# Kernel tuning notes

Hardware: AMD Instinct MI355X
Metric: run time of the kernel (lower is better)

## Reference

```python
import jax, jax.numpy as jnp
import numpy as np

B = 4096; NA = 32; DIU = 128; DOU = 32; DIB = 256; DOB = 64; DH = 128; N = NA + 1


def setup_inputs() -> dict:
    key = jax.random.key(0)
    ks = jax.random.split(key, 40)
    kidx = [0]
    def rn(shape, scale=0.1):
        k = ks[kidx[0]]; kidx[0] += 1
        return jax.random.normal(k, shape, jnp.float32) * scale
    inp = {}
    inp['s'] = rn((B, DIU * NA + DIB), 1.0)
    inp['a'] = rn((B, DOU * NA + DOB), 1.0)
    for pre, din in (('ue', DIU + DOU), ('bs', DIB + DOB)):
        inp[pre + '_l1_w'] = rn((din, DH))
        inp[pre + '_l1_b'] = jnp.zeros((DH,), jnp.float32)
        inp[pre + '_l2_w'] = rn((DH, DH))
        inp[pre + '_l2_b'] = jnp.zeros((DH,), jnp.float32)
        for l in range(2):
            inp[pre + f'_gru_wih{l}'] = rn((3 * DH, DH))
            inp[pre + f'_gru_whh{l}'] = rn((3 * DH, DH))
            inp[pre + f'_gru_bih{l}'] = jnp.zeros((3 * DH,), jnp.float32)
            inp[pre + f'_gru_bhh{l}'] = jnp.zeros((3 * DH,), jnp.float32)
    inp['gat_w'] = rn((DH, DH))
    inp['gat_a'] = rn((2 * DH, 1))
    adj = np.zeros((N, N), np.float32)
    adj[1:, 0] = 1.0
    adj[0, 1:] = 1.0  # star graph, as in generate_adjacent_matrix
    inp['adj'] = jnp.asarray(adj)
    inp['ev1_w'] = rn((DH, DH))
    inp['ev1_b'] = jnp.zeros((DH,), jnp.float32)
    inp['ev2_w'] = rn((DH, 1))
    inp['ev2_b'] = jnp.zeros((1,), jnp.float32)
    return inp


def _gru_layer(x, wih, whh, bih, bhh):
    # x: [B, T, H]; torch GRU gate order (r, z, n), weights [3H, H]
    h0 = jnp.zeros((x.shape[0], whh.shape[1]), x.dtype)
    def step(h, xt):
        gi = xt @ wih.T + bih
        gh = h @ whh.T + bhh
        ir, iz, inn = jnp.split(gi, 3, axis=-1)
        hr, hz, hn = jnp.split(gh, 3, axis=-1)
        r = jax.nn.sigmoid(ir + hr)
        z = jax.nn.sigmoid(iz + hz)
        n = jnp.tanh(inn + r * hn)
        h_new = (1.0 - z) * n + z * h
        return h_new, h_new
    _, ys = jax.lax.scan(step, h0, jnp.swapaxes(x, 0, 1))
    return jnp.swapaxes(ys, 0, 1)


def _critic(si, ai, l1w, l1b, l2w, l2b, g0, g1):
    x = jax.nn.relu(jnp.concatenate([si, ai], axis=-1) @ l1w + l1b)
    x = jax.nn.sigmoid(x @ l2w + l2b)
    x = _gru_layer(x, *g0)
    x = _gru_layer(x, *g1)
    return x


def reference(s, a,
              ue_l1_w, ue_l1_b, ue_l2_w, ue_l2_b,
              ue_gru_wih0, ue_gru_whh0, ue_gru_bih0, ue_gru_bhh0,
              ue_gru_wih1, ue_gru_whh1, ue_gru_bih1, ue_gru_bhh1,
              bs_l1_w, bs_l1_b, bs_l2_w, bs_l2_b,
              bs_gru_wih0, bs_gru_whh0, bs_gru_bih0, bs_gru_bhh0,
              bs_gru_wih1, bs_gru_whh1, bs_gru_bih1, bs_gru_bhh1,
              gat_w, gat_a, adj, ev1_w, ev1_b, ev2_w, ev2_b):
    batch = s.shape[0]
    s_ue = s[:, :DIU * NA].reshape(batch, NA, DIU)
    s_bs = s[:, DIU * NA:].reshape(batch, 1, DIB)
    a_ue = a[:, :DOU * NA].reshape(batch, NA, DOU)
    a_bs = a[:, -DOB:].reshape(batch, 1, DOB)
    emb_ue = _critic(s_ue, a_ue, ue_l1_w, ue_l1_b, ue_l2_w, ue_l2_b,
                     (ue_gru_wih0, ue_gru_whh0, ue_gru_bih0, ue_gru_bhh0),
                     (ue_gru_wih1, ue_gru_whh1, ue_gru_bih1, ue_gru_bhh1))
    emb_bs = _critic(s_bs, a_bs, bs_l1_w, bs_l1_b, bs_l2_w, bs_l2_b,
                     (bs_gru_wih0, bs_gru_whh0, bs_gru_bih0, bs_gru_bhh0),
                     (bs_gru_wih1, bs_gru_whh1, bs_gru_bih1, bs_gru_bhh1))
    emb = jnp.concatenate([emb_ue, emb_bs], axis=1)  # [B, N, DH]
    # GAT layer
    Wh = emb @ gat_w                                  # [B, N, DH]
    Wh1 = Wh @ gat_a[:DH]                             # [B, N, 1]
    Wh2 = Wh @ gat_a[DH:]                             # [B, N, 1]
    e = jax.nn.leaky_relu(Wh1 + jnp.swapaxes(Wh2, 1, 2), negative_slope=0.01)
    att = jnp.where(adj > 0, e, jnp.float32(-9e15))
    att = jax.nn.softmax(att, axis=1)                 # NOTE: dim=1, as in source
    # dropout is identity in eval mode
    h_prime = jnp.einsum('bij,bjf->bf', att, Wh)      # matmul + sum over dim 1
    h_prime = jax.nn.elu(h_prime)
    x = jax.nn.relu(h_prime @ ev1_w + ev1_b)
    return x @ ev2_w + ev2_b                          # [B, 1]
```

## Files before the change

kernel.cpp:

```cpp
#include <hip/hip_runtime.h>


typedef unsigned short u16;
typedef __bf16  bf16x8  __attribute__((ext_vector_type(8)));
typedef short   short8  __attribute__((ext_vector_type(8)));
typedef u16     u16x4   __attribute__((ext_vector_type(4)));
typedef float   floatx4 __attribute__((ext_vector_type(4)));

#define DEVI __device__ __forceinline__
#define MFMA(a, b, c) __builtin_amdgcn_mfma_f32_16x16x32_bf16((a), (b), (c), 0, 0, 0)

DEVI u16 f2b(float f) {
    unsigned u = __float_as_uint(f);
    u += 0x7fffu + ((u >> 16) & 1u);
    return (u16)(u >> 16);
}
DEVI float b2f(u16 s) { return __uint_as_float(((unsigned)s) << 16); }
DEVI float sigm(float x) { return 1.f / (1.f + __expf(-x)); }
DEVI float tanh_(float x) { return 1.f - 2.f / (__expf(2.f * x) + 1.f); }

DEVI bf16x8 ldfrag(const u16* q) {
    return *reinterpret_cast<const bf16x8*>(q);
}
DEVI bf16x8 ldfrag_f32(const float* q) {
    float4 u = *reinterpret_cast<const float4*>(q);
    float4 v = *reinterpret_cast<const float4*>(q + 4);
    short8 pk;
    pk[0] = (short)f2b(u.x); pk[1] = (short)f2b(u.y);
    pk[2] = (short)f2b(u.z); pk[3] = (short)f2b(u.w);
    pk[4] = (short)f2b(v.x); pk[5] = (short)f2b(v.y);
    pk[6] = (short)f2b(v.z); pk[7] = (short)f2b(v.w);
    return __builtin_bit_cast(bf16x8, pk);
}

enum : int {
    O_UE_W1T  = 0,
    O_UE_W2T  = 20480,
    O_UE_WIH0 = 36864,
    O_UE_WHH0 = 86016,
    O_UE_WIH1 = 135168,
    O_UE_WHH1 = 184320,
    O_BS_W1T  = 233472,
    O_BS_W2T  = 274432,
    O_BS_WIH0 = 290816,
    O_BS_WIH1 = 339968,
    O_GATWT   = 389120,
    O_EV1T    = 405504,
};
#define WB_X2   1048576u
#define WB_Y0   34603008u
#define WB_X2BS 135266304u
#define WB_H0BS 136314880u
#define WB_HBS  137363456u
#define WB_SSUM 139460608u

__global__ __launch_bounds__(256) void k_prep(
    const float* __restrict__ ue1, const float* __restrict__ ue2,
    const float* __restrict__ uw0, const float* __restrict__ uh0,
    const float* __restrict__ uw1, const float* __restrict__ uh1,
    const float* __restrict__ bs1, const float* __restrict__ bs2,
    const float* __restrict__ bw0, const float* __restrict__ bw1,
    const float* __restrict__ gw,  const float* __restrict__ e1,
    u16* __restrict__ out)
{
    const int tid = blockIdx.x * blockDim.x + threadIdx.x;
    const int stride = gridDim.x * blockDim.x;
    auto cvt = [&](const float* s, int off, int n) {
        for (int i = tid; i < n; i += stride) out[off + i] = f2b(s[i]);
    };
    auto tcv = [&](const float* s, int off, int K, int N) {
        const int tot = K * N;
        for (int i = tid; i < tot; i += stride) {
            int nn = i / K, kk = i - nn * K;
            out[off + i] = f2b(s[kk * N + nn]);
        }
    };
    tcv(ue1, O_UE_W1T, 160, 128);  tcv(ue2, O_UE_W2T, 128, 128);
    cvt(uw0, O_UE_WIH0, 49152);    cvt(uh0, O_UE_WHH0, 49152);
    cvt(uw1, O_UE_WIH1, 49152);    cvt(uh1, O_UE_WHH1, 49152);
    tcv(bs1, O_BS_W1T, 320, 128);  tcv(bs2, O_BS_W2T, 128, 128);
    cvt(bw0, O_BS_WIH0, 49152);    cvt(bw1, O_BS_WIH1, 49152);
    tcv(gw,  O_GATWT, 128, 128);   tcv(e1,  O_EV1T, 128, 128);
}

__global__ __launch_bounds__(512, 2) void k_ue_l1l2(
    const float* __restrict__ s, const float* __restrict__ a,
    const u16* __restrict__ W1T, const float* __restrict__ b1,
    const u16* __restrict__ W2T, const float* __restrict__ b2,
    u16* __restrict__ X2)
{
    __shared__ __align__(16) u16 A1[128][168];
    __shared__ __align__(16) u16 H[128][136];
    const int tid = threadIdx.x;
    const int w = tid >> 6, lane = tid & 63;
    const int lm = lane & 15, lg = lane >> 4;
    const int r0 = blockIdx.x * 128;

    bf16x8 bw1[5], bw2[4];
#pragma unroll
    for (int ks = 0; ks < 5; ++ks)
        bw1[ks] = ldfrag(W1T + (w * 16 + lm) * 160 + ks * 32 + lg * 8);
#pragma unroll
    for (int ks = 0; ks < 4; ++ks)
        bw2[ks] = ldfrag(W2T + (w * 16 + lm) * 128 + ks * 32 + lg * 8);
    const float bias1 = b1[w * 16 + lm];
    const float bias2 = b2[w * 16 + lm];

#pragma unroll
    for (int it = 0; it < 8; ++it) {
        const int fidx = it * 512 + tid;
        const int row = fidx >> 5, c4 = fidx & 31;
        const int r = r0 + row, bb = r >> 5, tt = r & 31;
        float4 v = *reinterpret_cast<const float4*>(s + (size_t)bb * 4352 + tt * 128 + c4 * 4);
        u16x4 p = {f2b(v.x), f2b(v.y), f2b(v.z), f2b(v.w)};
        *reinterpret_cast<u16x4*>(&A1[row][c4 * 4]) = p;
    }
#pragma unroll
    for (int it = 0; it < 2; ++it) {
        const int fidx = it * 512 + tid;
        const int row = fidx >> 3, c4 = fidx & 7;
        const int r = r0 + row, bb = r >> 5, tt = r & 31;
        float4 v = *reinterpret_cast<const float4*>(a + (size_t)bb * 1088 + tt * 32 + c4 * 4);
        u16x4 p = {f2b(v.x), f2b(v.y), f2b(v.z), f2b(v.w)};
        *reinterpret_cast<u16x4*>(&A1[row][128 + c4 * 4]) = p;
    }
    __syncthreads();

#pragma unroll
    for (int mt = 0; mt < 8; ++mt) {
        bf16x8 af[5];
#pragma unroll
        for (int ks = 0; ks < 5; ++ks)
            af[ks] = ldfrag(&A1[mt * 16 + lm][ks * 32 + lg * 8]);
        floatx4 acc = {0.f, 0.f, 0.f, 0.f};
#pragma unroll
        for (int ks = 0; ks < 5; ++ks) acc = MFMA(af[ks], bw1[ks], acc);
#pragma unroll
        for (int i = 0; i < 4; ++i) {
            float x = acc[i] + bias1;
            H[mt * 16 + lg * 4 + i][w * 16 + lm] = f2b(x > 0.f ? x : 0.f);
        }
    }
    __syncthreads();

#pragma unroll
    for (int mt = 0; mt < 8; ++mt) {
        bf16x8 af[4];
#pragma unroll
        for (int ks = 0; ks < 4; ++ks)
            af[ks] = ldfrag(&H[mt * 16 + lm][ks * 32 + lg * 8]);
        floatx4 acc = {0.f, 0.f, 0.f, 0.f};
#pragma unroll
        for (int ks = 0; ks < 4; ++ks) acc = MFMA(af[ks], bw2[ks], acc);
#pragma unroll
        for (int i = 0; i < 4; ++i)
            X2[(size_t)(r0 + mt * 16 + lg * 4 + i) * 128 + w * 16 + lm] =
                f2b(sigm(acc[i] + bias2));
    }
}

template <int MODE>
__global__ __launch_bounds__(512, 2) void k_scan(
    const u16* __restrict__ X, const u16* __restrict__ WIH,
    const u16* __restrict__ WHH,
    const float* __restrict__ bih, const float* __restrict__ bhh,
    u16* __restrict__ Y, float* __restrict__ Ssum)
{
    __shared__ __align__(16) u16 hb[2][16][136];
    const int w = threadIdx.x >> 6, lane = threadIdx.x & 63;
    const int lm = lane & 15, lg = lane >> 4;
    const int b0 = blockIdx.x * 16;
    const int c = w * 16 + lm;

    bf16x8 bwh[3][4], bwi[3][4];
#pragma unroll
    for (int g = 0; g < 3; ++g)
#pragma unroll
        for (int ks = 0; ks < 4; ++ks) {
            bwh[g][ks] = ldfrag(WHH + (g * 128 + c) * 128 + ks * 32 + lg * 8);
            bwi[g][ks] = ldfrag(WIH + (g * 128 + c) * 128 + ks * 32 + lg * 8);
        }

    for (int i = threadIdx.x; i < 2 * 16 * 136; i += 512) ((u16*)hb)[i] = 0;

    const float br  = bih[c] + bhh[c];
    const float bz  = bih[128 + c] + bhh[128 + c];
    const float bni = bih[256 + c], bnh = bhh[256 + c];

    const u16* xp = X + (size_t)(b0 + lm) * 32 * 128 + lg * 8;
    bf16x8 xa[4], xn[4];
#pragma unroll
    for (int ks = 0; ks < 4; ++ks) xa[ks] = ldfrag(xp + ks * 32);

    float hreg[4] = {}, ssum[4] = {};
    __syncthreads();

    int cur = 0;
    for (int t = 0; t < 32; ++t) {
        bf16x8 af[4];
#pragma unroll
        for (int ks = 0; ks < 4; ++ks)
            af[ks] = ldfrag(&hb[cur][lm][ks * 32 + lg * 8]);

        floatx4 gacc[3];
#pragma unroll
        for (int g = 0; g < 3; ++g) gacc[g] = floatx4{0.f, 0.f, 0.f, 0.f};
#pragma unroll
        for (int g = 0; g < 3; ++g)
#pragma unroll
            for (int ks = 0; ks < 4; ++ks)
                gacc[g] = MFMA(xa[ks], bwi[g][ks], gacc[g]);

        if (t < 31) {
#pragma unroll
            for (int ks = 0; ks < 4; ++ks)
                xn[ks] = ldfrag(xp + (t + 1) * 128 + ks * 32);
        }

        floatx4 hacc[3];
#pragma unroll
        for (int g = 0; g < 3; ++g) hacc[g] = floatx4{0.f, 0.f, 0.f, 0.f};
#pragma unroll
        for (int g = 0; g < 3; ++g)
#pragma unroll
            for (int ks = 0; ks < 4; ++ks)
                hacc[g] = MFMA(af[ks], bwh[g][ks], hacc[g]);

        const int nxt = cur ^ 1;
#pragma unroll
        for (int i = 0; i < 4; ++i) {
            const float rr = sigm(gacc[0][i] + hacc[0][i] + br);
            const float zz = sigm(gacc[1][i] + hacc[1][i] + bz);
            const float nn = tanh_(gacc[2][i] + bni + rr * (hacc[2][i] + bnh));
            const float hn = (1.f - zz) * nn + zz * hreg[i];
            hreg[i] = hn;
            if (MODE == 1) ssum[i] += hn;
            const u16 hv = f2b(hn);
            hb[nxt][lg * 4 + i][c] = hv;
            if (MODE == 0)
                Y[((size_t)(b0 + lg * 4 + i) * 32 + t) * 128 + c] = hv;
        }
#pragma unroll
        for (int ks = 0; ks < 4; ++ks) xa[ks] = xn[ks];

        __builtin_amdgcn_sched_barrier(0);
        asm volatile("s_waitcnt lgkmcnt(0)" ::: "memory");
        __builtin_amdgcn_s_barrier();
        __builtin_amdgcn_sched_barrier(0);
        cur = nxt;
    }
    if (MODE == 1) {
#pragma unroll
        for (int i = 0; i < 4; ++i)
            Ssum[(size_t)(b0 + lg * 4 + i) * 128 + c] = ssum[i];
    }
}

__global__ __launch_bounds__(256, 2) void k_bs_l1l2(
    const float* __restrict__ s, const float* __restrict__ a,
    const u16* __restrict__ W1T, const float* __restrict__ b1,
    const u16* __restrict__ W2T, const float* __restrict__ b2,
    u16* __restrict__ X2)
{
    __shared__ __align__(16) u16 hb[4][16][136];
    const int w = threadIdx.x >> 6, lane = threadIdx.x & 63;
    const int lm = lane & 15, lg = lane >> 4;
    const int r0 = blockIdx.x * 64 + w * 16;
    const float* srow = s + (size_t)(r0 + lm) * 4352 + 4096 + lg * 8;
    const float* arow = a + (size_t)(r0 + lm) * 1088 + 1024 + lg * 8;

    bf16x8 af[10];
#pragma unroll
    for (int ks = 0; ks < 8; ++ks) af[ks] = ldfrag_f32(srow + ks * 32);
    af[8] = ldfrag_f32(arow);
    af[9] = ldfrag_f32(arow + 32);

    const u16* wb1 = W1T + lm * 320 + lg * 8;
#pragma unroll
    for (int n = 0; n < 8; ++n) {
        floatx4 acc = {0.f, 0.f, 0.f, 0.f};
#pragma unroll
        for (int ks = 0; ks < 10; ++ks)
            acc = MFMA(af[ks], ldfrag(wb1 + n * 5120 + ks * 32), acc);
        const float bias = b1[n * 16 + lm];
#pragma unroll
        for (int i = 0; i < 4; ++i) {
            float x = acc[i] + bias;
            hb[w][lg * 4 + i][n * 16 + lm] = f2b(x > 0.f ? x : 0.f);
        }
    }
    __syncthreads();

    bf16x8 af2[4];
#pragma unroll
    for (int ks = 0; ks < 4; ++ks) af2[ks] = ldfrag(&hb[w][lm][ks * 32 + lg * 8]);
    const u16* wb2 = W2T + lm * 128 + lg * 8;
#pragma unroll
    for (int n = 0; n < 8; ++n) {
        floatx4 acc = {0.f, 0.f, 0.f, 0.f};
#pragma unroll
        for (int ks = 0; ks < 4; ++ks)
            acc = MFMA(af2[ks], ldfrag(wb2 + n * 2048 + ks * 32), acc);
        const float bias = b2[n * 16 + lm];
#pragma unroll
        for (int i = 0; i < 4; ++i) {
            float v = sigm(acc[i] + bias);
            X2[(unsigned)(r0 + lg * 4 + i) * 128u + n * 16 + lm] = f2b(v);
        }
    }
}

template <int OUTF32>
__global__ __launch_bounds__(256, 2) void k_bs_gru(
    const u16* __restrict__ X, const u16* __restrict__ WIH,
    const float* __restrict__ bih, const float* __restrict__ bhh,
    u16* __restrict__ Hb, float* __restrict__ Hf)
{
    const int w = threadIdx.x >> 6, lane = threadIdx.x & 63;
    const int lm = lane & 15, lg = lane >> 4;
    const int r0 = blockIdx.x * 64 + w * 16;

    bf16x8 ax[4];
    const u16* xr = X + (unsigned)(r0 + lm) * 128u + lg * 8;
#pragma unroll
    for (int ks = 0; ks < 4; ++ks) ax[ks] = ldfrag(xr + ks * 32);

    floatx4 acc[24];
#pragma unroll
    for (int j = 0; j < 24; ++j) acc[j] = floatx4{0.f, 0.f, 0.f, 0.f};
    const u16* wbp = WIH + lm * 128 + lg * 8;
#pragma unroll
    for (int j = 0; j < 24; ++j)
#pragma unroll
        for (int ks = 0; ks < 4; ++ks)
            acc[j] = MFMA(ax[ks], ldfrag(wbp + j * 2048 + ks * 32), acc[j]);

#pragma unroll
    for (int ct = 0; ct < 8; ++ct) {
        const int c = ct * 16 + lm;
        const float br = bih[c] + bhh[c];
        const float bz = bih[128 + c] + bhh[128 + c];
        const float bni = bih[256 + c], bnh = bhh[256 + c];
#pragma unroll
        for (int i = 0; i < 4; ++i) {
            const float rr = sigm(acc[ct][i] + br);
            const float zz = sigm(acc[8 + ct][i] + bz);
            const float nn = tanh_(acc[16 + ct][i] + bni + rr * bnh);
            const float h = (1.f - zz) * nn;
            const unsigned row = (unsigned)(r0 + lg * 4 + i);
            if (OUTF32) Hf[row * 128u + c] = h;
            else        Hb[row * 128u + c] = f2b(h);
        }
    }
}

__global__ __launch_bounds__(256, 2) void k_final(
    const float* __restrict__ Ssum, const float* __restrict__ HBS,
    const u16* __restrict__ GATWT, const u16* __restrict__ EV1T,
    const float* __restrict__ ev1b, const float* __restrict__ ev2w,
    const float* __restrict__ ev2b, float* __restrict__ out)
{
    __shared__ __align__(16) u16 hb[4][16][136];
    __shared__ float xb[4][16][132];
    const int w = threadIdx.x >> 6, lane = threadIdx.x & 63;
    const int lm = lane & 15, lg = lane >> 4;
    const int r0 = blockIdx.x * 64 + w * 16;

    const float* p1 = Ssum + (unsigned)(r0 + lm) * 128u + lg * 8;
    const float* p2 = HBS  + (unsigned)(r0 + lm) * 128u + lg * 8;
    bf16x8 af[4];
#pragma unroll
    for (int ks = 0; ks < 4; ++ks) {
        float4 u = *reinterpret_cast<const float4*>(p1 + ks * 32);
        float4 u2 = *reinterpret_cast<const float4*>(p1 + ks * 32 + 4);
        float4 v = *reinterpret_cast<const float4*>(p2 + ks * 32);
        float4 v2 = *reinterpret_cast<const float4*>(p2 + ks * 32 + 4);
        short8 pk;
        pk[0] = (short)f2b(u.x + v.x); pk[1] = (short)f2b(u.y + v.y);
        pk[2] = (short)f2b(u.z + v.z); pk[3] = (short)f2b(u.w + v.w);
        pk[4] = (short)f2b(u2.x + v2.x); pk[5] = (short)f2b(u2.y + v2.y);
        pk[6] = (short)f2b(u2.z + v2.z); pk[7] = (short)f2b(u2.w + v2.w);
        af[ks] = __builtin_bit_cast(bf16x8, pk);
    }
    const u16* gwp = GATWT + lm * 128 + lg * 8;
#pragma unroll
    for (int n = 0; n < 8; ++n) {
        floatx4 acc = {0.f, 0.f, 0.f, 0.f};
#pragma unroll
        for (int ks = 0; ks < 4; ++ks)
            acc = MFMA(af[ks], ldfrag(gwp + n * 2048 + ks * 32), acc);
#pragma unroll
        for (int i = 0; i < 4; ++i) {
            float x = acc[i];
            x = x > 0.f ? x : (__expf(x) - 1.f);
            hb[w][lg * 4 + i][n * 16 + lm] = f2b(x);
        }
    }
    __syncthreads();

    bf16x8 af2[4];
#pragma unroll
    for (int ks = 0; ks < 4; ++ks) af2[ks] = ldfrag(&hb[w][lm][ks * 32 + lg * 8]);
    const u16* e1p = EV1T + lm * 128 + lg * 8;
#pragma unroll
    for (int n = 0; n < 8; ++n) {
        floatx4 acc = {0.f, 0.f, 0.f, 0.f};
#pragma unroll
        for (int ks = 0; ks < 4; ++ks)
            acc = MFMA(af2[ks], ldfrag(e1p + n * 2048 + ks * 32), acc);
        const float bias = ev1b[n * 16 + lm];
#pragma unroll
        for (int i = 0; i < 4; ++i) {
            float v = acc[i] + bias;
            xb[w][lg * 4 + i][n * 16 + lm] = v > 0.f ? v : 0.f;
        }
    }
    __syncthreads();

    float sacc = 0.f;
#pragma unroll
    for (int k = 0; k < 32; ++k) {
        const int c = lg * 32 + k;
        sacc += xb[w][lm][c] * ev2w[c];
    }
    sacc += __shfl_xor(sacc, 16, 64);
    sacc += __shfl_xor(sacc, 32, 64);
    if (lg == 0) out[r0 + lm] = sacc + ev2b[0];
}

extern "C" void kernel_launch(void* const* d_in, const int* in_sizes, int n_in,
                              void* d_out, int out_size, void* d_ws, size_t ws_size,
                              hipStream_t stream)
{
    (void)in_sizes; (void)n_in; (void)out_size; (void)ws_size;
    const float* s       = (const float*)d_in[0];
    const float* a       = (const float*)d_in[1];
    const float* ue_l1_w = (const float*)d_in[2];
    const float* ue_l1_b = (const float*)d_in[3];
    const float* ue_l2_w = (const float*)d_in[4];
    const float* ue_l2_b = (const float*)d_in[5];
    const float* ue_wih0 = (const float*)d_in[6];
    const float* ue_whh0 = (const float*)d_in[7];
    const float* ue_bih0 = (const float*)d_in[8];
    const float* ue_bhh0 = (const float*)d_in[9];
    const float* ue_wih1 = (const float*)d_in[10];
    const float* ue_whh1 = (const float*)d_in[11];
    const float* ue_bih1 = (const float*)d_in[12];
    const float* ue_bhh1 = (const float*)d_in[13];
    const float* bs_l1_w = (const float*)d_in[14];
    const float* bs_l1_b = (const float*)d_in[15];
    const float* bs_l2_w = (const float*)d_in[16];
    const float* bs_l2_b = (const float*)d_in[17];
    const float* bs_wih0 = (const float*)d_in[18];
    const float* bs_bih0 = (const float*)d_in[20];
    const float* bs_bhh0 = (const float*)d_in[21];
    const float* bs_wih1 = (const float*)d_in[22];
    const float* bs_bih1 = (const float*)d_in[24];
    const float* bs_bhh1 = (const float*)d_in[25];
    const float* gat_w   = (const float*)d_in[26];
    const float* ev1_w   = (const float*)d_in[29];
    const float* ev1_b   = (const float*)d_in[30];
    const float* ev2_w   = (const float*)d_in[31];
    const float* ev2_b   = (const float*)d_in[32];

    char* ws = (char*)d_ws;
    u16*   wb   = (u16*)ws;
    u16*   X2   = (u16*)(ws + WB_X2);
    u16*   Y0   = (u16*)(ws + WB_Y0);
    u16*   X2BS = (u16*)(ws + WB_X2BS);
    u16*   H0BS = (u16*)(ws + WB_H0BS);
    float* HBS  = (float*)(ws + WB_HBS);
    float* SSUM = (float*)(ws + WB_SSUM);

    k_prep<<<256, 256, 0, stream>>>(ue_l1_w, ue_l2_w, ue_wih0, ue_whh0,
                                    ue_wih1, ue_whh1, bs_l1_w, bs_l2_w,
                                    bs_wih0, bs_wih1, gat_w, ev1_w, wb);
    k_ue_l1l2<<<1024, 512, 0, stream>>>(s, a, wb + O_UE_W1T, ue_l1_b,
                                        wb + O_UE_W2T, ue_l2_b, X2);
    k_scan<0><<<256, 512, 0, stream>>>(X2, wb + O_UE_WIH0, wb + O_UE_WHH0,
                                       ue_bih0, ue_bhh0, Y0, nullptr);
    k_scan<1><<<256, 512, 0, stream>>>(Y0, wb + O_UE_WIH1, wb + O_UE_WHH1,
                                       ue_bih1, ue_bhh1, nullptr, SSUM);
    k_bs_l1l2<<<64, 256, 0, stream>>>(s, a, wb + O_BS_W1T, bs_l1_b,
                                      wb + O_BS_W2T, bs_l2_b, X2BS);
    k_bs_gru<0><<<64, 256, 0, stream>>>(X2BS, wb + O_BS_WIH0, bs_bih0, bs_bhh0,
                                        H0BS, nullptr);
    k_bs_gru<1><<<64, 256, 0, stream>>>(H0BS, wb + O_BS_WIH1, bs_bih1, bs_bhh1,
                                        nullptr, HBS);
    k_final<<<64, 256, 0, stream>>>(SSUM, HBS, wb + O_GATWT, wb + O_EV1T,
                                    ev1_b, ev2_w, ev2_b, (float*)d_out);
}
```

Measured before the change: 370.6 us.

## Fuse BS critic kernels into final kernel and restructure GRU scan step

Merges the four small BS-path kernels (l1/l2, two single-step GRU layers, final GAT/eval head) into one kernel that keeps intermediates in shared memory instead of round-tripping through global workspace, removing three launches. The scan loop is manually unrolled by two with static ping-pong LDS buffers, input and hidden MFMAs accumulate into shared r/z accumulators, and s_setprio wraps the MFMA section. The added x prefetch depth and shared-memory reuse raise register and LDS pressure and need careful barrier placement.

New measurement: 359.3 us. -3.0%, faster.

```diff
diff --git a/kernel.cpp b/kernel.cpp
--- a/kernel.cpp
+++ b/kernel.cpp
@@ -49,9 +49,6 @@
 };
 #define WB_X2   1048576u
 #define WB_Y0   34603008u
-#define WB_X2BS 135266304u
-#define WB_H0BS 136314880u
-#define WB_HBS  137363456u
 #define WB_SSUM 139460608u
 
 __global__ __launch_bounds__(256) void k_prep(
@@ -159,6 +156,47 @@
     }
 }
 
+#define SCAN_STEP(RBUF, WBUF, XA, TCUR, PREF_T)                               \
+  {                                                                           \
+    bf16x8 af[4];                                                             \
+    _Pragma("unroll") for (int ks = 0; ks < 4; ++ks)                          \
+        af[ks] = ldfrag(&RBUF[lm][ks * 32 + lg * 8]);                         \
+    floatx4 accR{0.f,0.f,0.f,0.f}, accZ{0.f,0.f,0.f,0.f};                     \
+    floatx4 accGN{0.f,0.f,0.f,0.f}, accHN{0.f,0.f,0.f,0.f};                   \
+    __builtin_amdgcn_s_setprio(1);                                            \
+    _Pragma("unroll") for (int ks = 0; ks < 4; ++ks) {                        \
+        accR  = MFMA(XA[ks], bwi[0][ks], accR);                               \
+        accZ  = MFMA(XA[ks], bwi[1][ks], accZ);                               \
+        accGN = MFMA(XA[ks], bwi[2][ks], accGN);                              \
+    }                                                                         \
+    if ((PREF_T) < 32) {                                                      \
+        _Pragma("unroll") for (int ks = 0; ks < 4; ++ks)                      \
+            XA[ks] = ldfrag(xp + (PREF_T) * 128 + ks * 32);                   \
+    }                                                                         \
+    _Pragma("unroll") for (int ks = 0; ks < 4; ++ks) {                        \
+        accR = MFMA(af[ks], bwh[0][ks], accR);                                \
+        accZ = MFMA(af[ks], bwh[1][ks], accZ);                                \
+        accHN = MFMA(af[ks], bwh[2][ks], accHN);                              \
+    }                                                                         \
+    __builtin_amdgcn_s_setprio(0);                                            \
+    _Pragma("unroll") for (int i = 0; i < 4; ++i) {                           \
+        const float rr = sigm(accR[i] + br);                                  \
+        const float zz = sigm(accZ[i] + bz);                                  \
+        const float nn = tanh_(accGN[i] + bni + rr * (accHN[i] + bnh));       \
+        const float hn = (1.f - zz) * nn + zz * hreg[i];                      \
+        hreg[i] = hn;                                                         \
+        if (MODE == 1) ssum[i] += hn;                                         \
+        const u16 hv = f2b(hn);                                               \
+        WBUF[lg * 4 + i][c] = hv;                                             \
+        if (MODE == 0)                                                        \
+            Y[((size_t)(b0 + lg * 4 + i) * 32 + (TCUR)) * 128 + c] = hv;      \
+    }                                                                         \
+    __builtin_amdgcn_sched_barrier(0);                                        \
+    asm volatile("s_waitcnt lgkmcnt(0)" ::: "memory");                        \
+    __builtin_amdgcn_s_barrier();                                             \
+    __builtin_amdgcn_sched_barrier(0);                                        \
+  }
+
 template <int MODE>
 __global__ __launch_bounds__(512, 2) void k_scan(
     const u16* __restrict__ X, const u16* __restrict__ WIH,
@@ -166,7 +204,8 @@
     const float* __restrict__ bih, const float* __restrict__ bhh,
     u16* __restrict__ Y, float* __restrict__ Ssum)
 {
-    __shared__ __align__(16) u16 hb[2][16][136];
+    __shared__ __align__(16) u16 hb0[16][136];
+    __shared__ __align__(16) u16 hb1[16][136];
     const int w = threadIdx.x >> 6, lane = threadIdx.x & 63;
     const int lm = lane & 15, lg = lane >> 4;
     const int b0 = blockIdx.x * 16;
@@ -181,73 +220,28 @@
             bwi[g][ks] = ldfrag(WIH + (g * 128 + c) * 128 + ks * 32 + lg * 8);
         }
 
-    for (int i = threadIdx.x; i < 2 * 16 * 136; i += 512) ((u16*)hb)[i] = 0;
+    for (int i = threadIdx.x; i < 16 * 136; i += 512) {
+        ((u16*)hb0)[i] = 0; ((u16*)hb1)[i] = 0;
+    }
 
     const float br  = bih[c] + bhh[c];
     const float bz  = bih[128 + c] + bhh[128 + c];
     const float bni = bih[256 + c], bnh = bhh[256 + c];
 
     const u16* xp = X + (size_t)(b0 + lm) * 32 * 128 + lg * 8;
-    bf16x8 xa[4], xn[4];
-#pragma unroll
-    for (int ks = 0; ks < 4; ++ks) xa[ks] = ldfrag(xp + ks * 32);
+    bf16x8 xa[4], xb[4];
+#pragma unroll
+    for (int ks = 0; ks < 4; ++ks) {
+        xa[ks] = ldfrag(xp + ks * 32);
+        xb[ks] = ldfrag(xp + 128 + ks * 32);
+    }
 
     float hreg[4] = {}, ssum[4] = {};
     __syncthreads();
 
-    int cur = 0;
-    for (int t = 0; t < 32; ++t) {
-        bf16x8 af[4];
-#pragma unroll
-        for (int ks = 0; ks < 4; ++ks)
-            af[ks] = ldfrag(&hb[cur][lm][ks * 32 + lg * 8]);
-
-        floatx4 gacc[3];
-#pragma unroll
-        for (int g = 0; g < 3; ++g) gacc[g] = floatx4{0.f, 0.f, 0.f, 0.f};
-#pragma unroll
-        for (int g = 0; g < 3; ++g)
-#pragma unroll
-            for (int ks = 0; ks < 4; ++ks)
-                gacc[g] = MFMA(xa[ks], bwi[g][ks], gacc[g]);
-
-        if (t < 31) {
-#pragma unroll
-            for (int ks = 0; ks < 4; ++ks)
-                xn[ks] = ldfrag(xp + (t + 1) * 128 + ks * 32);
-        }
-
-        floatx4 hacc[3];
-#pragma unroll
-        for (int g = 0; g < 3; ++g) hacc[g] = floatx4{0.f, 0.f, 0.f, 0.f};
-#pragma unroll
-        for (int g = 0; g < 3; ++g)
-#pragma unroll
-            for (int ks = 0; ks < 4; ++ks)
-                hacc[g] = MFMA(af[ks], bwh[g][ks], hacc[g]);
-
-        const int nxt = cur ^ 1;
-#pragma unroll
-        for (int i = 0; i < 4; ++i) {
-            const float rr = sigm(gacc[0][i] + hacc[0][i] + br);
-            const float zz = sigm(gacc[1][i] + hacc[1][i] + bz);
-            const float nn = tanh_(gacc[2][i] + bni + rr * (hacc[2][i] + bnh));
-            const float hn = (1.f - zz) * nn + zz * hreg[i];
-            hreg[i] = hn;
-            if (MODE == 1) ssum[i] += hn;
-            const u16 hv = f2b(hn);
-            hb[nxt][lg * 4 + i][c] = hv;
-            if (MODE == 0)
-                Y[((size_t)(b0 + lg * 4 + i) * 32 + t) * 128 + c] = hv;
-        }
-#pragma unroll
-        for (int ks = 0; ks < 4; ++ks) xa[ks] = xn[ks];
-
-        __builtin_amdgcn_sched_barrier(0);
-        asm volatile("s_waitcnt lgkmcnt(0)" ::: "memory");
-        __builtin_amdgcn_s_barrier();
-        __builtin_amdgcn_sched_barrier(0);
-        cur = nxt;
+    for (int tt = 0; tt < 32; tt += 2) {
+        SCAN_STEP(hb0, hb1, xa, tt,     tt + 2);
+        SCAN_STEP(hb1, hb0, xb, tt + 1, tt + 3);
     }
     if (MODE == 1) {
 #pragma unroll
@@ -256,176 +250,202 @@
     }
 }
 
-__global__ __launch_bounds__(256, 2) void k_bs_l1l2(
+__global__ __launch_bounds__(256, 2) void k_bs_final(
     const float* __restrict__ s, const float* __restrict__ a,
     const u16* __restrict__ W1T, const float* __restrict__ b1,
     const u16* __restrict__ W2T, const float* __restrict__ b2,
-    u16* __restrict__ X2)
-{
-    __shared__ __align__(16) u16 hb[4][16][136];
-    const int w = threadIdx.x >> 6, lane = threadIdx.x & 63;
-    const int lm = lane & 15, lg = lane >> 4;
-    const int r0 = blockIdx.x * 64 + w * 16;
-    const float* srow = s + (size_t)(r0 + lm) * 4352 + 4096 + lg * 8;
-    const float* arow = a + (size_t)(r0 + lm) * 1088 + 1024 + lg * 8;
-
-    bf16x8 af[10];
-#pragma unroll
-    for (int ks = 0; ks < 8; ++ks) af[ks] = ldfrag_f32(srow + ks * 32);
-    af[8] = ldfrag_f32(arow);
-    af[9] = ldfrag_f32(arow + 32);
-
-    const u16* wb1 = W1T + lm * 320 + lg * 8;
-#pragma unroll
-    for (int n = 0; n < 8; ++n) {
-        floatx4 acc = {0.f, 0.f, 0.f, 0.f};
-#pragma unroll
-        for (int ks = 0; ks < 10; ++ks)
-            acc = MFMA(af[ks], ldfrag(wb1 + n * 5120 + ks * 32), acc);
-        const float bias = b1[n * 16 + lm];
-#pragma unroll
-        for (int i = 0; i < 4; ++i) {
-            float x = acc[i] + bias;
-            hb[w][lg * 4 + i][n * 16 + lm] = f2b(x > 0.f ? x : 0.f);
-        }
-    }
-    __syncthreads();
-
-    bf16x8 af2[4];
-#pragma unroll
-    for (int ks = 0; ks < 4; ++ks) af2[ks] = ldfrag(&hb[w][lm][ks * 32 + lg * 8]);
-    const u16* wb2 = W2T + lm * 128 + lg * 8;
-#pragma unroll
-    for (int n = 0; n < 8; ++n) {
-        floatx4 acc = {0.f, 0.f, 0.f, 0.f};
-#pragma unroll
-        for (int ks = 0; ks < 4; ++ks)
-            acc = MFMA(af2[ks], ldfrag(wb2 + n * 2048 + ks * 32), acc);
-        const float bias = b2[n * 16 + lm];
-#pragma unroll
-        for (int i = 0; i < 4; ++i) {
-            float v = sigm(acc[i] + bias);
-            X2[(unsigned)(r0 + lg * 4 + i) * 128u + n * 16 + lm] = f2b(v);
-        }
-    }
-}
-
-template <int OUTF32>
-__global__ __launch_bounds__(256, 2) void k_bs_gru(
-    const u16* __restrict__ X, const u16* __restrict__ WIH,
-    const float* __restrict__ bih, const float* __restrict__ bhh,
-    u16* __restrict__ Hb, float* __restrict__ Hf)
-{
-    const int w = threadIdx.x >> 6, lane = threadIdx.x & 63;
-    const int lm = lane & 15, lg = lane >> 4;
-    const int r0 = blockIdx.x * 64 + w * 16;
-
-    bf16x8 ax[4];
-    const u16* xr = X + (unsigned)(r0 + lm) * 128u + lg * 8;
-#pragma unroll
-    for (int ks = 0; ks < 4; ++ks) ax[ks] = ldfrag(xr + ks * 32);
-
-    floatx4 acc[24];
-#pragma unroll
-    for (int j = 0; j < 24; ++j) acc[j] = floatx4{0.f, 0.f, 0.f, 0.f};
-    const u16* wbp = WIH + lm * 128 + lg * 8;
-#pragma unroll
-    for (int j = 0; j < 24; ++j)
-#pragma unroll
-        for (int ks = 0; ks < 4; ++ks)
-            acc[j] = MFMA(ax[ks], ldfrag(wbp + j * 2048 + ks * 32), acc[j]);
-
-#pragma unroll
-    for (int ct = 0; ct < 8; ++ct) {
-        const int c = ct * 16 + lm;
-        const float br = bih[c] + bhh[c];
-        const float bz = bih[128 + c] + bhh[128 + c];
-        const float bni = bih[256 + c], bnh = bhh[256 + c];
-#pragma unroll
-        for (int i = 0; i < 4; ++i) {
-            const float rr = sigm(acc[ct][i] + br);
-            const float zz = sigm(acc[8 + ct][i] + bz);
-            const float nn = tanh_(acc[16 + ct][i] + bni + rr * bnh);
-            const float h = (1.f - zz) * nn;
-            const unsigned row = (unsigned)(r0 + lg * 4 + i);
-            if (OUTF32) Hf[row * 128u + c] = h;
-            else        Hb[row * 128u + c] = f2b(h);
-        }
-    }
-}
-
-__global__ __launch_bounds__(256, 2) void k_final(
-    const float* __restrict__ Ssum, const float* __restrict__ HBS,
+    const u16* __restrict__ WIH0, const float* __restrict__ bih0,
+    const float* __restrict__ bhh0,
+    const u16* __restrict__ WIH1, const float* __restrict__ bih1,
+    const float* __restrict__ bhh1,
+    const float* __restrict__ Ssum,
     const u16* __restrict__ GATWT, const u16* __restrict__ EV1T,
     const float* __restrict__ ev1b, const float* __restrict__ ev2w,
     const float* __restrict__ ev2b, float* __restrict__ out)
 {
-    __shared__ __align__(16) u16 hb[4][16][136];
-    __shared__ float xb[4][16][132];
+    __shared__ __align__(16) char smem[52224];
+    u16   (*X2L)[136] = reinterpret_cast<u16(*)[136]>(smem);
+    u16   (*HBP)[136] = reinterpret_cast<u16(*)[136]>(smem + 17408);
+    u16   (*H0L)[136] = reinterpret_cast<u16(*)[136]>(smem + 34816);
+    float (*HL)[132]  = reinterpret_cast<float(*)[132]>(smem);
+    u16   (*HBF)[136] = reinterpret_cast<u16(*)[136]>(smem + 34816);
+    float (*XBF)[132] = reinterpret_cast<float(*)[132]>(smem);
+
     const int w = threadIdx.x >> 6, lane = threadIdx.x & 63;
     const int lm = lane & 15, lg = lane >> 4;
     const int r0 = blockIdx.x * 64 + w * 16;
-
-    const float* p1 = Ssum + (unsigned)(r0 + lm) * 128u + lg * 8;
-    const float* p2 = HBS  + (unsigned)(r0 + lm) * 128u + lg * 8;
-    bf16x8 af[4];
-#pragma unroll
-    for (int ks = 0; ks < 4; ++ks) {
-        float4 u = *reinterpret_cast<const float4*>(p1 + ks * 32);
-        float4 u2 = *reinterpret_cast<const float4*>(p1 + ks * 32 + 4);
-        float4 v = *reinterpret_cast<const float4*>(p2 + ks * 32);
-        float4 v2 = *reinterpret_cast<const float4*>(p2 + ks * 32 + 4);
-        short8 pk;
-        pk[0] = (short)f2b(u.x + v.x); pk[1] = (short)f2b(u.y + v.y);
-        pk[2] = (short)f2b(u.z + v.z); pk[3] = (short)f2b(u.w + v.w);
-        pk[4] = (short)f2b(u2.x + v2.x); pk[5] = (short)f2b(u2.y + v2.y);
-        pk[6] = (short)f2b(u2.z + v2.z); pk[7] = (short)f2b(u2.w + v2.w);
-        af[ks] = __builtin_bit_cast(bf16x8, pk);
-    }
-    const u16* gwp = GATWT + lm * 128 + lg * 8;
-#pragma unroll
-    for (int n = 0; n < 8; ++n) {
-        floatx4 acc = {0.f, 0.f, 0.f, 0.f};
+    const int lr = w * 16;
+
+    {
+        const float* srow = s + (size_t)(r0 + lm) * 4352 + 4096 + lg * 8;
+        const float* arow = a + (size_t)(r0 + lm) * 1088 + 1024 + lg * 8;
+        bf16x8 af[10];
+#pragma unroll
+        for (int ks = 0; ks < 8; ++ks) af[ks] = ldfrag_f32(srow + ks * 32);
+        af[8] = ldfrag_f32(arow);
+        af[9] = ldfrag_f32(arow + 32);
+
+        const u16* wb1 = W1T + lm * 320 + lg * 8;
+#pragma unroll
+        for (int n = 0; n < 8; ++n) {
+            floatx4 acc = {0.f, 0.f, 0.f, 0.f};
+#pragma unroll
+            for (int ks = 0; ks < 10; ++ks)
+                acc = MFMA(af[ks], ldfrag(wb1 + n * 5120 + ks * 32), acc);
+            const float bias = b1[n * 16 + lm];
+#pragma unroll
+            for (int i = 0; i < 4; ++i) {
+                float x = acc[i] + bias;
+                HBP[lr + lg * 4 + i][n * 16 + lm] = f2b(x > 0.f ? x : 0.f);
+            }
+        }
+        __syncthreads();
+
+        bf16x8 af2[4];
 #pragma unroll
         for (int ks = 0; ks < 4; ++ks)
-            acc = MFMA(af[ks], ldfrag(gwp + n * 2048 + ks * 32), acc);
-#pragma unroll
-        for (int i = 0; i < 4; ++i) {
-            float x = acc[i];
-            x = x > 0.f ? x : (__expf(x) - 1.f);
-            hb[w][lg * 4 + i][n * 16 + lm] = f2b(x);
+            af2[ks] = ldfrag(&HBP[lr + lm][ks * 32 + lg * 8]);
+        const u16* wb2 = W2T + lm * 128 + lg * 8;
+#pragma unroll
+        for (int n = 0; n < 8; ++n) {
+            floatx4 acc = {0.f, 0.f, 0.f, 0.f};
+#pragma unroll
+            for (int ks = 0; ks < 4; ++ks)
+                acc = MFMA(af2[ks], ldfrag(wb2 + n * 2048 + ks * 32), acc);
+            const float bias = b2[n * 16 + lm];
+#pragma unroll
+            for (int i = 0; i < 4; ++i)
+                X2L[lr + lg * 4 + i][n * 16 + lm] = f2b(sigm(acc[i] + bias));
         }
     }
     __syncthreads();
 
-    bf16x8 af2[4];
-#pragma unroll
-    for (int ks = 0; ks < 4; ++ks) af2[ks] = ldfrag(&hb[w][lm][ks * 32 + lg * 8]);
-    const u16* e1p = EV1T + lm * 128 + lg * 8;
-#pragma unroll
-    for (int n = 0; n < 8; ++n) {
-        floatx4 acc = {0.f, 0.f, 0.f, 0.f};
+    {
+        bf16x8 ax[4];
 #pragma unroll
         for (int ks = 0; ks < 4; ++ks)
-            acc = MFMA(af2[ks], ldfrag(e1p + n * 2048 + ks * 32), acc);
-        const float bias = ev1b[n * 16 + lm];
-#pragma unroll
-        for (int i = 0; i < 4; ++i) {
-            float v = acc[i] + bias;
-            xb[w][lg * 4 + i][n * 16 + lm] = v > 0.f ? v : 0.f;
+            ax[ks] = ldfrag(&X2L[lr + lm][ks * 32 + lg * 8]);
+        floatx4 acc[24];
+#pragma unroll
+        for (int j = 0; j < 24; ++j) acc[j] = floatx4{0.f, 0.f, 0.f, 0.f};
+        const u16* wbp = WIH0 + lm * 128 + lg * 8;
+#pragma unroll
+        for (int j = 0; j < 24; ++j)
+#pragma unroll
+            for (int ks = 0; ks < 4; ++ks)
+                acc[j] = MFMA(ax[ks], ldfrag(wbp + j * 2048 + ks * 32), acc[j]);
+#pragma unroll
+        for (int ct = 0; ct < 8; ++ct) {
+            const int cc = ct * 16 + lm;
+            const float brr = bih0[cc] + bhh0[cc];
+            const float bzz = bih0[128 + cc] + bhh0[128 + cc];
+            const float bni = bih0[256 + cc], bnh = bhh0[256 + cc];
+#pragma unroll
+            for (int i = 0; i < 4; ++i) {
+                const float rr = sigm(acc[ct][i] + brr);
+                const float zz = sigm(acc[8 + ct][i] + bzz);
+                const float nn = tanh_(acc[16 + ct][i] + bni + rr * bnh);
+                H0L[lr + lg * 4 + i][cc] = f2b((1.f - zz) * nn);
+            }
         }
     }
     __syncthreads();
 
-    float sacc = 0.f;
-#pragma unroll
-    for (int k = 0; k < 32; ++k) {
-        const int c = lg * 32 + k;
-        sacc += xb[w][lm][c] * ev2w[c];
-    }
-    sacc += __shfl_xor(sacc, 16, 64);
-    sacc += __shfl_xor(sacc, 32, 64);
-    if (lg == 0) out[r0 + lm] = sacc + ev2b[0];
+    {
+        bf16x8 ax[4];
+#pragma unroll
+        for (int ks = 0; ks < 4; ++ks)
+            ax[ks] = ldfrag(&H0L[lr + lm][ks * 32 + lg * 8]);
+        floatx4 acc[24];
+#pragma unroll
+        for (int j = 0; j < 24; ++j) acc[j] = floatx4{0.f, 0.f, 0.f, 0.f};
+        const u16* wbp = WIH1 + lm * 128 + lg * 8;
+#pragma unroll
+        for (int j = 0; j < 24; ++j)
+#pragma unroll
+            for (int ks = 0; ks < 4; ++ks)
+                acc[j] = MFMA(ax[ks], ldfrag(wbp + j * 2048 + ks * 32), acc[j]);
+        __syncthreads();
+#pragma unroll
+        for (int ct = 0; ct < 8; ++ct) {
+            const int cc = ct * 16 + lm;
+            const float brr = bih1[cc] + bhh1[cc];
+            const float bzz = bih1[128 + cc] + bhh1[128 + cc];
+            const float bni = bih1[256 + cc], bnh = bhh1[256 + cc];
+#pragma unroll
+            for (int i = 0; i < 4; ++i) {
+                const float rr = sigm(acc[ct][i] + brr);
+                const float zz = sigm(acc[8 + ct][i] + bzz);
+                const float nn = tanh_(acc[16 + ct][i] + bni + rr * bnh);
+                HL[lr + lg * 4 + i][cc] = (1.f - zz) * nn;
+            }
+        }
+    }
+    __syncthreads();
+
+    {
+        const float* p1 = Ssum + (size_t)(r0 + lm) * 128 + lg * 8;
+        bf16x8 af[4];
+#pragma unroll
+        for (int ks = 0; ks < 4; ++ks) {
+            float4 u  = *reinterpret_cast<const float4*>(p1 + ks * 32);
+            float4 u2 = *reinterpret_cast<const float4*>(p1 + ks * 32 + 4);
+            float4 v  = *reinterpret_cast<const float4*>(&HL[lr + lm][ks * 32 + lg * 8]);
+            float4 v2 = *reinterpret_cast<const float4*>(&HL[lr + lm][ks * 32 + lg * 8 + 4]);
+            short8 pk;
+            pk[0] = (short)f2b(u.x + v.x);  pk[1] = (short)f2b(u.y + v.y);
+            pk[2] = (short)f2b(u.z + v.z);  pk[3] = (short)f2b(u.w + v.w);
+            pk[4] = (short)f2b(u2.x + v2.x); pk[5] = (short)f2b(u2.y + v2.y);
+            pk[6] = (short)f2b(u2.z + v2.z); pk[7] = (short)f2b(u2.w + v2.w);
+            af[ks] = __builtin_bit_cast(bf16x8, pk);
+        }
+        __syncthreads();
+        const u16* gwp = GATWT + lm * 128 + lg * 8;
+#pragma unroll
+        for (int n = 0; n < 8; ++n) {
+            floatx4 acc = {0.f, 0.f, 0.f, 0.f};
+#pragma unroll
+            for (int ks = 0; ks < 4; ++ks)
+                acc = MFMA(af[ks], ldfrag(gwp + n * 2048 + ks * 32), acc);
+#pragma unroll
+            for (int i = 0; i < 4; ++i) {
+                float x = acc[i];
+                x = x > 0.f ? x : (__expf(x) - 1.f);
+                HBF[lr + lg * 4 + i][n * 16 + lm] = f2b(x);
+            }
+        }
+        __syncthreads();
+
+        bf16x8 af2[4];
+#pragma unroll
+        for (int ks = 0; ks < 4; ++ks)
+            af2[ks] = ldfrag(&HBF[lr + lm][ks * 32 + lg * 8]);
+        const u16* e1p = EV1T + lm * 128 + lg * 8;
+#pragma unroll
+        for (int n = 0; n < 8; ++n) {
+            floatx4 acc = {0.f, 0.f, 0.f, 0.f};
+#pragma unroll
+            for (int ks = 0; ks < 4; ++ks)
+                acc = MFMA(af2[ks], ldfrag(e1p + n * 2048 + ks * 32), acc);
+            const float bias = ev1b[n * 16 + lm];
+#pragma unroll
+            for (int i = 0; i < 4; ++i) {
+                float v = acc[i] + bias;
+                XBF[lr + lg * 4 + i][n * 16 + lm] = v > 0.f ? v : 0.f;
+            }
+        }
+        __syncthreads();
+
+        float sacc = 0.f;
+#pragma unroll
+        for (int k = 0; k < 32; ++k) {
+            const int cc = lg * 32 + k;
+            sacc += XBF[lr + lm][cc] * ev2w[cc];
+        }
+        sacc += __shfl_xor(sacc, 16, 64);
+        sacc += __shfl_xor(sacc, 32, 64);
+        if (lg == 0) out[r0 + lm] = sacc + ev2b[0];
+    }
 }
 
 extern "C" void kernel_launch(void* const* d_in, const int* in_sizes, int n_in,
@@ -467,9 +487,6 @@
     u16*   wb   = (u16*)ws;
     u16*   X2   = (u16*)(ws + WB_X2);
     u16*   Y0   = (u16*)(ws + WB_Y0);
-    u16*   X2BS = (u16*)(ws + WB_X2BS);
-    u16*   H0BS = (u16*)(ws + WB_H0BS);
-    float* HBS  = (float*)(ws + WB_HBS);
     float* SSUM = (float*)(ws + WB_SSUM);
 
     k_prep<<<256, 256, 0, stream>>>(ue_l1_w, ue_l2_w, ue_wih0, ue_whh0,
@@ -481,12 +498,10 @@
                                        ue_bih0, ue_bhh0, Y0, nullptr);
     k_scan<1><<<256, 512, 0, stream>>>(Y0, wb + O_UE_WIH1, wb + O_UE_WHH1,
                                        ue_bih1, ue_bhh1, nullptr, SSUM);
-    k_bs_l1l2<<<64, 256, 0, stream>>>(s, a, wb + O_BS_W1T, bs_l1_b,
-                                      wb + O_BS_W2T, bs_l2_b, X2BS);
-    k_bs_gru<0><<<64, 256, 0, stream>>>(X2BS, wb + O_BS_WIH0, bs_bih0, bs_bhh0,
-                                        H0BS, nullptr);
-    k_bs_gru<1><<<64, 256, 0, stream>>>(H0BS, wb + O_BS_WIH1, bs_bih1, bs_bhh1,
-                                        nullptr, HBS);
-    k_final<<<64, 256, 0, stream>>>(SSUM, HBS, wb + O_GATWT, wb + O_EV1T,
-                                    ev1_b, ev2_w, ev2_b, (float*)d_out);
-}
+    k_bs_final<<<64, 256, 0, stream>>>(s, a, wb + O_BS_W1T, bs_l1_b,
+                                       wb + O_BS_W2T, bs_l2_b,
+                                       wb + O_BS_WIH0, bs_bih0, bs_bhh0,
+                                       wb + O_BS_WIH1, bs_bih1, bs_bhh1,
+                                       SSUM, wb + O_GATWT, wb + O_EV1T,
+                                       ev1_b, ev2_w, ev2_b, (float*)d_out);
+}
```
